# Performance work log

Measured on AMD Instinct MI355X. Metric: run time of the kernel, lower is better.

Reference implementation:

```python
import jax, jax.numpy as jnp
import numpy as np

SIZE = 7
SIGMA = 1.5
K1 = 0.01
K2 = 0.03
DATA_RANGE = 2.0
NP_ = SIZE * SIZE
COV_NORM = NP_ / (NP_ - 1)
PAD = SIZE // 2


def _gaussian_window(size=SIZE, sigma=SIGMA, channels=1):
    x = np.arange(size) - size // 2
    g = np.exp(-x**2 / (2.0 * sigma**2))[None, :]
    g = (g.T @ g)
    g = g / g.sum()
    w = np.tile(g[None, None], (channels, 1, 1, 1))  # [C,1,size,size]
    return jnp.asarray(w, dtype=jnp.float32)


def _dwconv(x, w):
    # depthwise conv2d, zero padding PAD, stride 1; x: [N,C,H,W], w: [C,1,k,k]
    c = x.shape[1]
    return jax.lax.conv_general_dilated(
        x, w, window_strides=(1, 1), padding=[(PAD, PAD), (PAD, PAD)],
        dimension_numbers=('NCHW', 'OIHW', 'NCHW'), feature_group_count=c)


def setup_inputs() -> dict:
    key = jax.random.key(0)
    k1, k2 = jax.random.split(key)
    X = jax.random.uniform(k1, (64, 1, 320, 320), dtype=jnp.float32)
    Y = jax.random.uniform(k2, (64, 1, 320, 320), dtype=jnp.float32)
    window = _gaussian_window()
    return {"X": X, "Y": Y, "window": window}


def reference(X, Y, window):
    C1 = (K1 * DATA_RANGE) ** 2
    C2 = (K2 * DATA_RANGE) ** 2
    mux = _dwconv(X, window)
    muy = _dwconv(Y, window)
    mux_sq = mux * mux
    muy_sq = muy * muy
    muxy = mux * muy
    sigmax_sq = (_dwconv(X * X, window) - mux_sq) * COV_NORM
    sigmay_sq = (_dwconv(Y * Y, window) - muy_sq) * COV_NORM
    sigmaxy = (_dwconv(X * Y, window) - muxy) * COV_NORM
    ssim_map = ((2 * muxy + C1) * (2 * sigmaxy + C2)) / \
               ((mux_sq + muy_sq + C1) * (sigmax_sq + sigmay_sq + C2))
    return 1.0 - ssim_map.mean()
```

## Files before the change

kernel.cpp:

```cpp
#include <hip/hip_runtime.h>
#include <math.h>


#define WI 320
#define HI 320
#define NI 64
#define TW 64
#define TH 32
#define GXD 5
#define GYD 10
#define NBLK (GXD * GYD * NI)
#define LSTR 72
#define NPIX ((double)NI * WI * HI)

typedef float v4 __attribute__((ext_vector_type(4)));

struct W7 { float w[7]; };

template <bool INTERIOR>
__device__ __forceinline__ void column_task(
    const float* __restrict__ Xn, const float* __restrict__ Yn,
    const W7& wv, float* __restrict__ vbuf, int tx0, int ty0, int band, int ci)
{
    const int gx  = tx0 + ci - 3;
    const bool xok = (unsigned)gx < (unsigned)WI;
    const int gy0 = ty0 + band * 8 - 3;

    float acc[5][8];
#pragma unroll
    for (int ch = 0; ch < 5; ++ch)
#pragma unroll
        for (int r = 0; r < 8; ++r) acc[ch][r] = 0.f;

#pragma unroll
    for (int j = 0; j < 14; ++j) {
        const int gy = gy0 + j;
        float xv = 0.f, yv = 0.f;
        const bool ok = INTERIOR ? xok : (xok && ((unsigned)gy < (unsigned)HI));
        if (ok) {
            int idx = gy * WI + gx;
            xv = Xn[idx];
            yv = Yn[idx];
        }
        const float pxx = xv * xv, pyy = yv * yv, pxy = xv * yv;
#pragma unroll
        for (int r = 0; r < 8; ++r) {
            const int d = j - r;
            if (d >= 0 && d < 7) {
                const float w = wv.w[d];
                acc[0][r] += w * xv;
                acc[1][r] += w * yv;
                acc[2][r] += w * pxx;
                acc[3][r] += w * pyy;
                acc[4][r] += w * pxy;
            }
        }
    }
#pragma unroll
    for (int ch = 0; ch < 5; ++ch)
#pragma unroll
        for (int r = 0; r < 8; ++r)
            vbuf[ch * (TH * LSTR) + (band * 8 + r) * LSTR + (ci + 1)] = acc[ch][r];
}

__global__ __launch_bounds__(256) void ssim_kernel(
    const float* __restrict__ X, const float* __restrict__ Y,
    W7 wv, float* __restrict__ partial)
{
    __shared__ __align__(16) float vbuf[5 * TH * LSTR];
    __shared__ float wsum[4];

    const int tid = threadIdx.x;
    const int tx0 = blockIdx.x * TW;
    const int ty0 = blockIdx.y * TH;
    const float* __restrict__ Xn = X + (size_t)blockIdx.z * (WI * HI);
    const float* __restrict__ Yn = Y + (size_t)blockIdx.z * (WI * HI);

    const bool interior = (blockIdx.y >= 1) && (blockIdx.y <= GYD - 2);
    if (interior) {
        column_task<true>(Xn, Yn, wv, vbuf, tx0, ty0, tid >> 6, tid & 63);
        if (tid < 24) column_task<true>(Xn, Yn, wv, vbuf, tx0, ty0, tid / 6, 64 + tid % 6);
    } else {
        column_task<false>(Xn, Yn, wv, vbuf, tx0, ty0, tid >> 6, tid & 63);
        if (tid < 24) column_task<false>(Xn, Yn, wv, vbuf, tx0, ty0, tid / 6, 64 + tid % 6);
    }
    __syncthreads();

    const float C1 = 0.0004f, C2 = 0.0036f, COVN = 49.f / 48.f;
    const int xg   = (tid & 15) << 2;
    const int row0 = tid >> 4;

    float lsum = 0.f;
#pragma unroll
    for (int pass = 0; pass < 2; ++pass) {
        const int row = row0 + pass * 16;
        float f[5][12];
#pragma unroll
        for (int ch = 0; ch < 5; ++ch) {
            const v4* p = (const v4*)&vbuf[ch * (TH * LSTR) + row * LSTR + xg];
            v4 a = p[0], b = p[1], c = p[2];
            f[ch][0] = a.x; f[ch][1] = a.y; f[ch][2]  = a.z; f[ch][3]  = a.w;
            f[ch][4] = b.x; f[ch][5] = b.y; f[ch][6]  = b.z; f[ch][7]  = b.w;
            f[ch][8] = c.x; f[ch][9] = c.y; f[ch][10] = c.z; f[ch][11] = c.w;
        }
#pragma unroll
        for (int j = 0; j < 4; ++j) {
            float mx = 0.f, my = 0.f, sxx = 0.f, syy = 0.f, sxy = 0.f;
#pragma unroll
            for (int d = 0; d < 7; ++d) {
                const float w = wv.w[d];
                mx  += w * f[0][j + d + 1];
                my  += w * f[1][j + d + 1];
                sxx += w * f[2][j + d + 1];
                syy += w * f[3][j + d + 1];
                sxy += w * f[4][j + d + 1];
            }
            const float mxsq = mx * mx;
            const float mysq = my * my;
            const float mxy  = mx * my;
            const float vx   = (sxx - mxsq) * COVN;
            const float vy   = (syy - mysq) * COVN;
            const float vxy  = (sxy - mxy)  * COVN;
            const float num  = (2.f * mxy + C1) * (2.f * vxy + C2);
            const float den  = (mxsq + mysq + C1) * (vx + vy + C2);
            lsum += num * __builtin_amdgcn_rcpf(den);
        }
    }

#pragma unroll
    for (int off = 32; off > 0; off >>= 1)
        lsum += __shfl_down(lsum, off, 64);
    if ((tid & 63) == 0) wsum[tid >> 6] = lsum;
    __syncthreads();
    if (tid == 0) {
        int bid = (blockIdx.z * GYD + blockIdx.y) * GXD + blockIdx.x;
        partial[bid] = (wsum[0] + wsum[1]) + (wsum[2] + wsum[3]);
    }
}

__global__ __launch_bounds__(256) void ssim_finalize(
    const float* __restrict__ partial, float* __restrict__ out)
{
    __shared__ double ws[4];
    const int tid = threadIdx.x;
    double s = 0.0;
    for (int i = tid; i < NBLK; i += 256) s += (double)partial[i];
#pragma unroll
    for (int off = 32; off > 0; off >>= 1)
        s += __shfl_down(s, off, 64);
    if ((tid & 63) == 0) ws[tid >> 6] = s;
    __syncthreads();
    if (tid == 0)
        out[0] = (float)(1.0 - ((ws[0] + ws[1]) + (ws[2] + ws[3])) / NPIX);
}

extern "C" void kernel_launch(void* const* d_in, const int* in_sizes, int n_in,
                              void* d_out, int out_size, void* d_ws, size_t ws_size,
                              hipStream_t stream) {
    const float* X = (const float*)d_in[0];
    const float* Y = (const float*)d_in[1];
    W7 wv;
    {
        double g[7], s = 0.0;
        for (int i = 0; i < 7; ++i) {
            double x = (double)(i - 3);
            g[i] = exp(-(x * x) / (2.0 * 1.5 * 1.5));
            s += g[i];
        }
        for (int i = 0; i < 7; ++i) wv.w[i] = (float)(g[i] / s);
    }

    float* partial = (float*)d_ws;

    dim3 grid(GXD, GYD, NI);
    ssim_kernel<<<grid, 256, 0, stream>>>(X, Y, wv, partial);
    ssim_finalize<<<1, 256, 0, stream>>>(partial, (float*)d_out);
}
```

Before: 114.6 us.

## Halve tile height, move halo columns to a fifth wave, restructure horizontal pass

Tile height drops from 32 to 16 rows, which doubles the grid, shrinks the vertical accumulator arrays from 8 to 4 rows, and halves the shared-memory tile. The block grows to 320 threads so the 24 halo-column tasks run on a dedicated fifth wave instead of serialising on wave 0. The horizontal pass now handles one row per thread and reduces each channel in turn to lower register pressure, with launch bounds asking for 7 waves per SIMD. In exchange, the vertical halo overhead per output row roughly grows (10 loads for 4 rows versus 14 for 8), and the fifth wave sits idle during the horizontal pass.

```diff
diff --git a/kernel.cpp b/kernel.cpp
--- a/kernel.cpp
+++ b/kernel.cpp
@@ -6,9 +6,9 @@
 #define HI 320
 #define NI 64
 #define TW 64
-#define TH 32
+#define TH 16
 #define GXD 5
-#define GYD 10
+#define GYD 20
 #define NBLK (GXD * GYD * NI)
 #define LSTR 72
 #define NPIX ((double)NI * WI * HI)
@@ -24,16 +24,16 @@
 {
     const int gx  = tx0 + ci - 3;
     const bool xok = (unsigned)gx < (unsigned)WI;
-    const int gy0 = ty0 + band * 8 - 3;
+    const int gy0 = ty0 + band * 4 - 3;
 
-    float acc[5][8];
+    float acc[5][4];
 #pragma unroll
     for (int ch = 0; ch < 5; ++ch)
 #pragma unroll
-        for (int r = 0; r < 8; ++r) acc[ch][r] = 0.f;
+        for (int r = 0; r < 4; ++r) acc[ch][r] = 0.f;
 
 #pragma unroll
-    for (int j = 0; j < 14; ++j) {
+    for (int j = 0; j < 10; ++j) {
         const int gy = gy0 + j;
         float xv = 0.f, yv = 0.f;
         const bool ok = INTERIOR ? xok : (xok && ((unsigned)gy < (unsigned)HI));
@@ -44,7 +44,7 @@
         }
         const float pxx = xv * xv, pyy = yv * yv, pxy = xv * yv;
 #pragma unroll
-        for (int r = 0; r < 8; ++r) {
+        for (int r = 0; r < 4; ++r) {
             const int d = j - r;
             if (d >= 0 && d < 7) {
                 const float w = wv.w[d];
@@ -59,16 +59,16 @@
 #pragma unroll
     for (int ch = 0; ch < 5; ++ch)
 #pragma unroll
-        for (int r = 0; r < 8; ++r)
-            vbuf[ch * (TH * LSTR) + (band * 8 + r) * LSTR + (ci + 1)] = acc[ch][r];
+        for (int r = 0; r < 4; ++r)
+            vbuf[ch * (TH * LSTR) + (band * 4 + r) * LSTR + ci] = acc[ch][r];
 }
 
-__global__ __launch_bounds__(256) void ssim_kernel(
+__global__ __launch_bounds__(320, 7) void ssim_kernel(
     const float* __restrict__ X, const float* __restrict__ Y,
     W7 wv, float* __restrict__ partial)
 {
     __shared__ __align__(16) float vbuf[5 * TH * LSTR];
-    __shared__ float wsum[4];
+    __shared__ float wsum[5];
 
     const int tid = threadIdx.x;
     const int tx0 = blockIdx.x * TW;
@@ -78,49 +78,56 @@
 
     const bool interior = (blockIdx.y >= 1) && (blockIdx.y <= GYD - 2);
     if (interior) {
-        column_task<true>(Xn, Yn, wv, vbuf, tx0, ty0, tid >> 6, tid & 63);
-        if (tid < 24) column_task<true>(Xn, Yn, wv, vbuf, tx0, ty0, tid / 6, 64 + tid % 6);
+        if (tid < 256) {
+            column_task<true>(Xn, Yn, wv, vbuf, tx0, ty0, tid >> 6, tid & 63);
+        } else if (tid < 280) {
+            const int e = tid - 256;
+            column_task<true>(Xn, Yn, wv, vbuf, tx0, ty0, e / 6, 64 + e % 6);
+        }
     } else {
-        column_task<false>(Xn, Yn, wv, vbuf, tx0, ty0, tid >> 6, tid & 63);
-        if (tid < 24) column_task<false>(Xn, Yn, wv, vbuf, tx0, ty0, tid / 6, 64 + tid % 6);
+        if (tid < 256) {
+            column_task<false>(Xn, Yn, wv, vbuf, tx0, ty0, tid >> 6, tid & 63);
+        } else if (tid < 280) {
+            const int e = tid - 256;
+            column_task<false>(Xn, Yn, wv, vbuf, tx0, ty0, e / 6, 64 + e % 6);
+        }
     }
     __syncthreads();
 
-    const float C1 = 0.0004f, C2 = 0.0036f, COVN = 49.f / 48.f;
-    const int xg   = (tid & 15) << 2;
-    const int row0 = tid >> 4;
+    float lsum = 0.f;
+    if (tid < 256) {
+        const float C1 = 0.0004f, C2 = 0.0036f, COVN = 49.f / 48.f;
+        const int row = tid >> 4;
+        const int xg  = (tid & 15) << 2;
 
-    float lsum = 0.f;
+        float m[4][5];
 #pragma unroll
-    for (int pass = 0; pass < 2; ++pass) {
-        const int row = row0 + pass * 16;
-        float f[5][12];
+        for (int j = 0; j < 4; ++j)
+#pragma unroll
+            for (int ch = 0; ch < 5; ++ch) m[j][ch] = 0.f;
+
 #pragma unroll
         for (int ch = 0; ch < 5; ++ch) {
             const v4* p = (const v4*)&vbuf[ch * (TH * LSTR) + row * LSTR + xg];
             v4 a = p[0], b = p[1], c = p[2];
-            f[ch][0] = a.x; f[ch][1] = a.y; f[ch][2]  = a.z; f[ch][3]  = a.w;
-            f[ch][4] = b.x; f[ch][5] = b.y; f[ch][6]  = b.z; f[ch][7]  = b.w;
-            f[ch][8] = c.x; f[ch][9] = c.y; f[ch][10] = c.z; f[ch][11] = c.w;
+            float f[12] = {a.x,a.y,a.z,a.w, b.x,b.y,b.z,b.w, c.x,c.y,c.z,c.w};
+#pragma unroll
+            for (int j = 0; j < 4; ++j) {
+                float s = 0.f;
+#pragma unroll
+                for (int d = 0; d < 7; ++d) s += wv.w[d] * f[j + d];
+                m[j][ch] = s;
+            }
         }
 #pragma unroll
         for (int j = 0; j < 4; ++j) {
-            float mx = 0.f, my = 0.f, sxx = 0.f, syy = 0.f, sxy = 0.f;
-#pragma unroll
-            for (int d = 0; d < 7; ++d) {
-                const float w = wv.w[d];
-                mx  += w * f[0][j + d + 1];
-                my  += w * f[1][j + d + 1];
-                sxx += w * f[2][j + d + 1];
-                syy += w * f[3][j + d + 1];
-                sxy += w * f[4][j + d + 1];
-            }
+            const float mx = m[j][0], my = m[j][1];
             const float mxsq = mx * mx;
             const float mysq = my * my;
             const float mxy  = mx * my;
-            const float vx   = (sxx - mxsq) * COVN;
-            const float vy   = (syy - mysq) * COVN;
-            const float vxy  = (sxy - mxy)  * COVN;
+            const float vx   = (m[j][2] - mxsq) * COVN;
+            const float vy   = (m[j][3] - mysq) * COVN;
+            const float vxy  = (m[j][4] - mxy)  * COVN;
             const float num  = (2.f * mxy + C1) * (2.f * vxy + C2);
             const float den  = (mxsq + mysq + C1) * (vx + vy + C2);
             lsum += num * __builtin_amdgcn_rcpf(den);
@@ -134,7 +141,7 @@
     __syncthreads();
     if (tid == 0) {
         int bid = (blockIdx.z * GYD + blockIdx.y) * GXD + blockIdx.x;
-        partial[bid] = (wsum[0] + wsum[1]) + (wsum[2] + wsum[3]);
+        partial[bid] = ((wsum[0] + wsum[1]) + (wsum[2] + wsum[3])) + wsum[4];
     }
 }
 
@@ -173,6 +180,6 @@
     float* partial = (float*)d_ws;
 
     dim3 grid(GXD, GYD, NI);
-    ssim_kernel<<<grid, 256, 0, stream>>>(X, Y, wv, partial);
+    ssim_kernel<<<grid, 320, 0, stream>>>(X, Y, wv, partial);
     ssim_finalize<<<1, 256, 0, stream>>>(partial, (float*)d_out);
 }
```

Result: slower. 136.7 us (+19.3%).
